# Performance work log

Measured on AMD Instinct MI355X. Metric: run time of the kernel, lower is better.

The kernel has to match this reference:

```python
import jax, jax.numpy as jnp
import numpy as np

N_ITERS = 30  # sinkhorn iterations, matching torch default


def sinkhorn(log_alpha, n_iters=N_ITERS):
    # log_alpha: (B, N, K) -> approximately doubly-stochastic (B, N, K)
    x = log_alpha - jnp.max(log_alpha, axis=(-2, -1), keepdims=True)
    x = jnp.exp(x)
    for _ in range(n_iters):
        x = x / (jnp.sum(x, axis=-1, keepdims=True) + 1e-8)  # row normalize
        x = x / (jnp.sum(x, axis=-2, keepdims=True) + 1e-8)  # col normalize
    return x


def greedy_unique_argmax(scores):
    # scores: (B, N, K) with N == K. Returns hard permutation matrix (B, N, K).
    B, N, K = scores.shape

    def one(s):  # s: (N, K)
        order = jnp.argsort(-s.reshape(-1))  # flat indices, descending score

        def body(carry, idx):
            used_r, used_c, assign = carry
            r = idx // K
            c = idx % K
            take = jnp.logical_not(used_r[r] | used_c[c])
            used_r = used_r.at[r].set(used_r[r] | take)
            used_c = used_c.at[c].set(used_c[c] | take)
            assign = assign.at[r].set(jnp.where(take, c, assign[r]))
            return (used_r, used_c, assign), None

        init = (jnp.zeros((N,), jnp.bool_),
                jnp.zeros((K,), jnp.bool_),
                jnp.full((N,), 0, jnp.int32))
        (_, _, assign), _ = jax.lax.scan(body, init, order)
        return jax.nn.one_hot(assign, K, dtype=s.dtype)

    return jax.vmap(one)(scores)


def setup_inputs() -> dict:
    key = jax.random.key(0)
    B, N, K = 4096, 64, 64
    cell_logits = jax.random.normal(key, (B, N, K), dtype=jnp.float32)
    pos_temp = jnp.asarray(1.1, dtype=jnp.float32)  # softplus(pos_temp_raw)+1e-6 at init
    return {"cell_logits": cell_logits, "pos_temp": pos_temp}


def reference(cell_logits, pos_temp):
    logits = cell_logits / (pos_temp + 1e-6)
    w_soft = sinkhorn(logits, N_ITERS)
    w_hard = greedy_unique_argmax(jax.lax.stop_gradient(w_soft))
    # straight-through: forward = hard permutation, backward = soft sinkhorn grads
    w = w_hard + (w_soft - jax.lax.stop_gradient(w_soft))
    return w
```

## Files before the change

### kernel.cpp

```cpp
#include <hip/hip_runtime.h>
#include <cstdint>
#include <cstddef>


__device__ __forceinline__ float rl(float x, int lane) {
    return __uint_as_float((unsigned)__builtin_amdgcn_readlane((int)__float_as_uint(x), lane));
}

#define RESCAN(G)                                                            \
  {                                                                          \
    float nv_ = -__builtin_inff(); int na_ = (G) * 8;                        \
    _Pragma("unroll")                                                        \
    for (int k_ = 0; k_ < 8; ++k_) {                                         \
      const int idx_ = (G) * 8 + k_;                                         \
      float vk_ = ((rowmask >> idx_) & 1ull) ? col[idx_]                     \
                                             : -__builtin_inff();            \
      if (vk_ > nv_) { nv_ = vk_; na_ = idx_; }                              \
    }                                                                        \
    gv[(G)] = nv_; ga[(G)] = na_;                                            \
  }

#define RESCAN_SWITCH(RG)                                                    \
    switch (RG) {                                                            \
        case 0: RESCAN(0) break;                                             \
        case 1: RESCAN(1) break;                                             \
        case 2: RESCAN(2) break;                                             \
        case 3: RESCAN(3) break;                                             \
        case 4: RESCAN(4) break;                                             \
        case 5: RESCAN(5) break;                                             \
        case 6: RESCAN(6) break;                                             \
        case 7: RESCAN(7) break;                                             \
    }

__global__ void __launch_bounds__(64, 2)
sinkhorn_perm_kernel(const float* __restrict__ logits,
                     const float* __restrict__ ptemp,
                     float* __restrict__ out)
{
    const int b    = blockIdx.x;
    const int lane = threadIdx.x;
    const float* base = logits + (size_t)b * 4096;

    const float T    = ptemp[0] + 1e-6f;
    const float invT = 1.0f / T;

    float row[64];
    {
        const float4* rp = (const float4*)(base + lane * 64);
        #pragma unroll
        for (int t = 0; t < 16; ++t) {
            float4 q = rp[t];
            row[4*t+0] = __fmul_rn(q.x, invT);
            row[4*t+1] = __fmul_rn(q.y, invT);
            row[4*t+2] = __fmul_rn(q.z, invT);
            row[4*t+3] = __fmul_rn(q.w, invT);
        }
    }

    float mx = row[0];
    #pragma unroll
    for (int i = 1; i < 64; ++i) mx = fmaxf(mx, row[i]);
    #pragma unroll
    for (int w = 1; w <= 32; w <<= 1)
        mx = fmaxf(mx, __shfl_xor(mx, w, 64));

    #pragma unroll
    for (int i = 0; i < 64; ++i)
        row[i] = __expf(__fsub_rn(row[i], mx));

    float col[64];
    #pragma unroll
    for (int i = 0; i < 64; ++i) {
        float raw = base[i * 64 + lane];
        col[i] = __expf(__fsub_rn(__fmul_rn(raw, invT), mx));
    }

    float u = 1.0f, v = 1.0f;
    for (int it = 0; it < 30; ++it) {
        float a0 = 0.f, a1 = 0.f, a2 = 0.f, a3 = 0.f;
        #pragma unroll
        for (int j = 0; j < 64; j += 4) {
            a0 = __builtin_fmaf(row[j+0], rl(v, j+0), a0);
            a1 = __builtin_fmaf(row[j+1], rl(v, j+1), a1);
            a2 = __builtin_fmaf(row[j+2], rl(v, j+2), a2);
            a3 = __builtin_fmaf(row[j+3], rl(v, j+3), a3);
        }
        float rs = __fadd_rn(__fadd_rn(a0, a1), __fadd_rn(a2, a3));
        u = u / __fadd_rn(__fmul_rn(u, rs), 1e-8f);

        a0 = a1 = a2 = a3 = 0.f;
        #pragma unroll
        for (int i = 0; i < 64; i += 4) {
            a0 = __builtin_fmaf(col[i+0], rl(u, i+0), a0);
            a1 = __builtin_fmaf(col[i+1], rl(u, i+1), a1);
            a2 = __builtin_fmaf(col[i+2], rl(u, i+2), a2);
            a3 = __builtin_fmaf(col[i+3], rl(u, i+3), a3);
        }
        float cs = __fadd_rn(__fadd_rn(a0, a1), __fadd_rn(a2, a3));
        v = v / __fadd_rn(__fmul_rn(v, cs), 1e-8f);
    }

    #pragma unroll
    for (int i = 0; i < 64; ++i)
        col[i] = __fmul_rn(__fmul_rn(col[i], rl(u, i)), v);

    unsigned long long rowmask = ~0ull;
    float gv[8]; int ga[8];
    #pragma unroll
    for (int g = 0; g < 8; ++g) RESCAN(g)

    int  mycol   = 0;
    bool done    = false;
    int  retired = 0;
    const float NEGINF = -__builtin_inff();

    while (retired < 64) {
        float bv = gv[0]; int ba = ga[0];
        #pragma unroll
        for (int g2 = 1; g2 < 8; ++g2)
            if (gv[g2] > bv) { bv = gv[g2]; ba = ga[g2]; }
        float mybv = done ? NEGINF : bv;

        float m1 = mybv, m2 = NEGINF;
        #pragma unroll
        for (int m = 1; m <= 32; m <<= 1) {
            float o1 = __shfl_xor(m1, m, 64);
            float o2 = __shfl_xor(m2, m, 64);
            float hi = fmaxf(m1, o1);
            float lo = fminf(m1, o1);
            m1 = hi;
            m2 = fmaxf(lo, fmaxf(m2, o2));
        }

        int r1, c1, r2 = -1, c2 = -1;
        bool two = false;
        unsigned long long t1 = __ballot(mybv == m1);
        bool fast1 = (__popcll(t1) == 1) && (m2 > NEGINF);

        if (fast1) {
            c1 = (int)__builtin_ctzll(t1);
            r1 = __builtin_amdgcn_readlane(ba, c1);
            unsigned long long t2 = __ballot(mybv == m2);
            if (__popcll(t2) == 1) {
                c2 = (int)__builtin_ctzll(t2);
                r2 = __builtin_amdgcn_readlane(ba, c2);
                two = (r2 != r1);
            }
        } else {
            unsigned flat = ((unsigned)ba << 6) | (unsigned)lane;
            unsigned long long key =
                ((unsigned long long)__float_as_uint(bv) << 12) | (4095u - flat);
            if (done) key = 0ull;
            #pragma unroll
            for (int m = 1; m <= 32; m <<= 1) {
                unsigned long long o = __shfl_xor(key, m, 64);
                if (o > key) key = o;
            }
            unsigned wflat = 4095u - (unsigned)(key & 4095ull);
            r1 = __builtin_amdgcn_readfirstlane((int)(wflat >> 6));
            c1 = (int)(wflat & 63u);
        }

        if (lane == r1) mycol = c1;
        if (lane == c1) done  = true;
        rowmask &= ~(1ull << r1);
        retired++;
        if (two) {
            if (lane == r2) mycol = c2;
            if (lane == c2) done  = true;
            rowmask &= ~(1ull << r2);
            retired++;
        }

        RESCAN_SWITCH(r1 >> 3)
        if (two && ((r2 >> 3) != (r1 >> 3))) {
            RESCAN_SWITCH(r2 >> 3)
        }
    }

    float* orow = out + (size_t)b * 4096 + lane * 64;
    #pragma unroll
    for (int t = 0; t < 16; ++t) {
        float4 q;
        q.x = (4*t+0 == mycol) ? 1.0f : 0.0f;
        q.y = (4*t+1 == mycol) ? 1.0f : 0.0f;
        q.z = (4*t+2 == mycol) ? 1.0f : 0.0f;
        q.w = (4*t+3 == mycol) ? 1.0f : 0.0f;
        ((float4*)orow)[t] = q;
    }
}

extern "C" void kernel_launch(void* const* d_in, const int* in_sizes, int n_in,
                              void* d_out, int out_size, void* d_ws, size_t ws_size,
                              hipStream_t stream) {
    const float* logits = (const float*)d_in[0];
    const float* ptemp  = (const float*)d_in[1];
    float* out = (float*)d_out;
    const int B = in_sizes[0] / 4096;
    sinkhorn_perm_kernel<<<B, 64, 0, stream>>>(logits, ptemp, out);
}
```

Measured before the change: 221.1 us.

## Drop row copy, compute row sums via butterfly transpose-reduce, pack 4 waves/block

Removes the 64-register row array so each lane holds only its column. Row sums are now computed with a recursive-halving shuffle reduction over col*v, in place of readlane-broadcast FMAs. The point is to halve register pressure so more waves fit per SIMD. It also launches 4 problems per 256-thread block. The cost is many more cross-lane shuffles (about 126 per iteration) and a different summation order, which can change rounding slightly.

```diff
diff --git a/kernel.cpp b/kernel.cpp
--- a/kernel.cpp
+++ b/kernel.cpp
@@ -32,63 +32,66 @@
         case 7: RESCAN(7) break;                                             \
     }
 
-__global__ void __launch_bounds__(64, 2)
+__global__ void __launch_bounds__(256)
 sinkhorn_perm_kernel(const float* __restrict__ logits,
                      const float* __restrict__ ptemp,
-                     float* __restrict__ out)
+                     float* __restrict__ out, int B)
 {
-    const int b    = blockIdx.x;
-    const int lane = threadIdx.x;
+    const int wid  = threadIdx.x >> 6;
+    const int lane = threadIdx.x & 63;
+    const int b    = blockIdx.x * 4 + wid;
+    if (b >= B) return;
+
     const float* base = logits + (size_t)b * 4096;
 
     const float T    = ptemp[0] + 1e-6f;
     const float invT = 1.0f / T;
 
-    float row[64];
-    {
-        const float4* rp = (const float4*)(base + lane * 64);
-        #pragma unroll
-        for (int t = 0; t < 16; ++t) {
-            float4 q = rp[t];
-            row[4*t+0] = __fmul_rn(q.x, invT);
-            row[4*t+1] = __fmul_rn(q.y, invT);
-            row[4*t+2] = __fmul_rn(q.z, invT);
-            row[4*t+3] = __fmul_rn(q.w, invT);
-        }
-    }
-
-    float mx = row[0];
-    #pragma unroll
-    for (int i = 1; i < 64; ++i) mx = fmaxf(mx, row[i]);
+    float col[64];
+    #pragma unroll
+    for (int i = 0; i < 64; ++i)
+        col[i] = __fmul_rn(base[i * 64 + lane], invT);
+
+    float mx = col[0];
+    #pragma unroll
+    for (int i = 1; i < 64; ++i) mx = fmaxf(mx, col[i]);
     #pragma unroll
     for (int w = 1; w <= 32; w <<= 1)
         mx = fmaxf(mx, __shfl_xor(mx, w, 64));
 
     #pragma unroll
     for (int i = 0; i < 64; ++i)
-        row[i] = __expf(__fsub_rn(row[i], mx));
-
-    float col[64];
-    #pragma unroll
-    for (int i = 0; i < 64; ++i) {
-        float raw = base[i * 64 + lane];
-        col[i] = __expf(__fsub_rn(__fmul_rn(raw, invT), mx));
-    }
+        col[i] = __expf(__fsub_rn(col[i], mx));
 
     float u = 1.0f, v = 1.0f;
     for (int it = 0; it < 30; ++it) {
+        float t[32];
+        {
+            const bool h32 = (lane & 32) != 0;
+            #pragma unroll
+            for (int s = 0; s < 32; ++s) {
+                float plo = __fmul_rn(col[s],      v);
+                float phi = __fmul_rn(col[s + 32], v);
+                float olo = __shfl_xor(plo, 32, 64);
+                float ohi = __shfl_xor(phi, 32, 64);
+                t[s] = __fadd_rn(h32 ? phi : plo, h32 ? ohi : olo);
+            }
+        }
+        #pragma unroll
+        for (int m = 16; m >= 1; m >>= 1) {
+            const bool hm = (lane & m) != 0;
+            #pragma unroll
+            for (int s = 0; s < m; ++s) {
+                float a   = hm ? t[s + m] : t[s];
+                float olo = __shfl_xor(t[s],     m, 64);
+                float ohi = __shfl_xor(t[s + m], m, 64);
+                t[s] = __fadd_rn(a, hm ? ohi : olo);
+            }
+        }
+        float r = t[0];
+        u = u / __fadd_rn(__fmul_rn(u, r), 1e-8f);
+
         float a0 = 0.f, a1 = 0.f, a2 = 0.f, a3 = 0.f;
-        #pragma unroll
-        for (int j = 0; j < 64; j += 4) {
-            a0 = __builtin_fmaf(row[j+0], rl(v, j+0), a0);
-            a1 = __builtin_fmaf(row[j+1], rl(v, j+1), a1);
-            a2 = __builtin_fmaf(row[j+2], rl(v, j+2), a2);
-            a3 = __builtin_fmaf(row[j+3], rl(v, j+3), a3);
-        }
-        float rs = __fadd_rn(__fadd_rn(a0, a1), __fadd_rn(a2, a3));
-        u = u / __fadd_rn(__fmul_rn(u, rs), 1e-8f);
-
-        a0 = a1 = a2 = a3 = 0.f;
         #pragma unroll
         for (int i = 0; i < 64; i += 4) {
             a0 = __builtin_fmaf(col[i+0], rl(u, i+0), a0);
@@ -180,13 +183,13 @@
 
     float* orow = out + (size_t)b * 4096 + lane * 64;
     #pragma unroll
-    for (int t = 0; t < 16; ++t) {
+    for (int t2 = 0; t2 < 16; ++t2) {
         float4 q;
-        q.x = (4*t+0 == mycol) ? 1.0f : 0.0f;
-        q.y = (4*t+1 == mycol) ? 1.0f : 0.0f;
-        q.z = (4*t+2 == mycol) ? 1.0f : 0.0f;
-        q.w = (4*t+3 == mycol) ? 1.0f : 0.0f;
-        ((float4*)orow)[t] = q;
+        q.x = (4*t2+0 == mycol) ? 1.0f : 0.0f;
+        q.y = (4*t2+1 == mycol) ? 1.0f : 0.0f;
+        q.z = (4*t2+2 == mycol) ? 1.0f : 0.0f;
+        q.w = (4*t2+3 == mycol) ? 1.0f : 0.0f;
+        ((float4*)orow)[t2] = q;
     }
 }
 
@@ -197,5 +200,5 @@
     const float* ptemp  = (const float*)d_in[1];
     float* out = (float*)d_out;
     const int B = in_sizes[0] / 4096;
-    sinkhorn_perm_kernel<<<B, 64, 0, stream>>>(logits, ptemp, out);
+    sinkhorn_perm_kernel<<<(B + 3) / 4, 256, 0, stream>>>(logits, ptemp, out, B);
 }
```

After: 728.7 us. 3.3x slower.
